# Kernel optimization log

Measured on AMD Instinct MI355X. Metric: run time of the kernel, lower is better.

## Reference

```python
import math
import jax, jax.numpy as jnp
import numpy as np

N_TOKENS = 131072
D_MODEL = 1024
NUM_EXPERT = 64
SWITCH_EPS = 0.1
CAP_RATE = 1.2  # training capacity factor


def setup_inputs() -> dict:
    key = jax.random.key(0)
    k1, k2, k3, k4 = jax.random.split(key, 4)
    inp = jax.random.normal(k1, (N_TOKENS, D_MODEL), dtype=jnp.float32)
    W = jax.random.normal(k2, (D_MODEL, NUM_EXPERT), dtype=jnp.float32) * (1.0 / math.sqrt(D_MODEL))
    b = jax.random.normal(k3, (NUM_EXPERT,), dtype=jnp.float32) * 0.01
    noise = jax.random.uniform(k4, (N_TOKENS, NUM_EXPERT), dtype=jnp.float32)
    return {"inp": inp, "W": W, "b": b, "noise": noise}


def reference(inp, W, b, noise):
    n_tokens = inp.shape[0]
    # gate projection + training-time noise injection (noise in [1-eps, 1+eps])
    score = inp @ W + b
    score = score + (noise * (2.0 * SWITCH_EPS) + (1.0 - SWITCH_EPS))
    score = jax.nn.softmax(score.astype(jnp.float32), axis=-1)  # [N, E]

    # top-1 selection
    top1_idx = jnp.argmax(score, axis=-1)  # [N] int
    top1_score = jnp.take_along_axis(score, top1_idx[:, None], axis=-1)  # [N, 1]
    top1_score = top1_score.astype(inp.dtype)

    # capacity-limited pruning: keep first `capacity` tokens per expert (in order)
    capacity = math.ceil(CAP_RATE * n_tokens / NUM_EXPERT)  # static
    onehot = jax.nn.one_hot(top1_idx, NUM_EXPERT, dtype=jnp.int32)  # [N, E]
    # rank of each token within its expert (0-based, tokens in arrival order)
    rank = jnp.sum(jnp.cumsum(onehot, axis=0) * onehot, axis=-1) - 1  # [N]
    pruned_idx = jnp.where(rank < capacity, top1_idx, -1)  # [N]

    # load-balancing loss over valid (non-pruned) assignments
    valid = pruned_idx > -1
    n_valid = jnp.sum(valid).astype(jnp.float32)
    safe_idx = jnp.where(valid, pruned_idx, 0)
    counts = jnp.zeros((NUM_EXPERT,), dtype=jnp.float32).at[safe_idx].add(valid.astype(jnp.float32))
    fraction_expert = counts / n_valid
    prob_expert = jnp.sum(score, axis=0) / n_valid
    loss = jnp.sum(fraction_expert * prob_expert) * NUM_EXPERT

    return pruned_idx[:, None], top1_score, loss
```

## Files before the change

kernel.cpp:

```cpp
#include <hip/hip_runtime.h>
#include <stdint.h>

#define NTOK   131072
#define DM     1024
#define NE     64
#define TB     64
#define NBLK   2048
#define BK     32
#define NCHUNK 32
#define CAP    2458
#define EPG    16

__device__ __forceinline__ void gload_lds16(const float* g, float* l) {
    __builtin_amdgcn_global_load_lds(
        (const __attribute__((address_space(1))) void*)g,
        (__attribute__((address_space(3))) void*)l, 16, 0, 0);
}

__global__ __launch_bounds__(256, 8)
void gate_kernel(const float* __restrict__ A, const float* __restrict__ W,
                 const float* __restrict__ bias, const float* __restrict__ noise,
                 float* __restrict__ out, int* __restrict__ pk,
                 int* __restrict__ histg, float* __restrict__ colpart)
{
    __shared__ float asA[2][TB][BK];
    __shared__ float smax[TB][5];
    __shared__ float ssum[TB][5];
    __shared__ int   sidx[TB][5];

    const int tid  = threadIdx.x;
    const int lane = tid & 63;
    const int wv   = __builtin_amdgcn_readfirstlane(tid >> 6);
    const int g16  = wv << 4;
    const int blk  = blockIdx.x;
    const int tokBase = blk * TB;
    const int token   = tokBase + lane;

    float acc[EPG];
#pragma unroll
    for (int e = 0; e < EPG; ++e) acc[e] = 0.f;

    const int sl = (lane & 7) ^ ((lane >> 3) & 7);
    const float* gsrc = A + (size_t)(tokBase + wv * 16 + (lane >> 3)) * DM + sl * 4;
    float* lb[2] = { &asA[0][wv * 16][0], &asA[1][wv * 16][0] };

    gload_lds16(gsrc,          lb[0]);
    gload_lds16(gsrc + 8 * DM, lb[0] + 8 * BK);
    __syncthreads();

#pragma unroll 1
    for (int c = 0; c < NCHUNK; ++c) {
        const int cur = c & 1;
        if (c + 1 < NCHUNK) {
            const float* gn = gsrc + (size_t)(c + 1) * BK;
            float* ln = lb[cur ^ 1];
            gload_lds16(gn,          ln);
            gload_lds16(gn + 8 * DM, ln + 8 * BK);
        }
        const float* arow = &asA[cur][lane][0];
        const int k0 = c * BK;
#pragma unroll
        for (int q = 0; q < 8; ++q) {
            const float4 xq = *(const float4*)(arow + ((q ^ (lane & 7)) << 2));
            const float xs[4] = {xq.x, xq.y, xq.z, xq.w};
#pragma unroll
            for (int kk = 0; kk < 4; ++kk) {
                const float x = xs[kk];
                const float* wrow = W + (size_t)(k0 + q * 4 + kk) * NE + g16;
#pragma unroll
                for (int e = 0; e < EPG; ++e)
                    acc[e] = fmaf(x, wrow[e], acc[e]);
            }
        }
        __syncthreads();
    }

    const float* nrow = noise + (size_t)token * NE + g16;
    const float* brow = bias + g16;
#pragma unroll
    for (int q = 0; q < 4; ++q) {
        const float4 nv = ((const float4*)nrow)[q];
        acc[q * 4 + 0] += brow[q * 4 + 0] + nv.x * 0.2f + 0.9f;
        acc[q * 4 + 1] += brow[q * 4 + 1] + nv.y * 0.2f + 0.9f;
        acc[q * 4 + 2] += brow[q * 4 + 2] + nv.z * 0.2f + 0.9f;
        acc[q * 4 + 3] += brow[q * 4 + 3] + nv.w * 0.2f + 0.9f;
    }

    float lm = acc[0]; int li = 0;
#pragma unroll
    for (int e = 1; e < EPG; ++e)
        if (acc[e] > lm) { lm = acc[e]; li = e; }
    smax[lane][wv] = lm;
    sidx[lane][wv] = g16 + li;
    __syncthreads();

    float M = smax[lane][0]; int bi = sidx[lane][0];
#pragma unroll
    for (int g2 = 1; g2 < 4; ++g2) {
        const float m2 = smax[lane][g2];
        if (m2 > M) { M = m2; bi = sidx[lane][g2]; }
    }

    float s = 0.f;
#pragma unroll
    for (int e = 0; e < EPG; ++e) { acc[e] = __expf(acc[e] - M); s += acc[e]; }
    ssum[lane][wv] = s;
    __syncthreads();
    const float denom = ssum[lane][0] + ssum[lane][1] + ssum[lane][2] + ssum[lane][3];
    const float inv = 1.0f / denom;
#pragma unroll
    for (int e = 0; e < EPG; ++e) acc[e] *= inv;

    if (wv == 0) out[NTOK + token] = inv;

#define XSTAGE(M_)                                                       \
    {                                                                    \
        const bool up_ = (lane & (M_)) != 0;                             \
        _Pragma("unroll")                                                \
        for (int j = 0; j < (M_); ++j) {                                 \
            const float a_ = acc[j], b_ = acc[j + (M_)];                 \
            const float r_ = __shfl_xor(up_ ? a_ : b_, (M_), 64);        \
            acc[j] = (up_ ? b_ : a_) + r_;                               \
        }                                                                \
    }
    XSTAGE(8) XSTAGE(4) XSTAGE(2) XSTAGE(1)
#undef XSTAGE
    float cs = acc[0];
    cs += __shfl_xor(cs, 16, 64);
    cs += __shfl_xor(cs, 32, 64);
    if (lane < EPG) colpart[blk * NE + g16 + lane] = cs;

    if (wv == 0) {
        const uint64_t below = (1ull << lane) - 1ull;
        int lrank = 0, h = 0;
#pragma unroll 1
        for (int e = 0; e < NE; ++e) {
            const uint64_t mb = __ballot(bi == e);
            if (bi == e)   lrank = (int)__popcll(mb & below);
            if (lane == e) h = (int)__popcll(mb);
        }
        pk[token] = bi | (lrank << 6);
        histg[blk * NE + lane] = h;
    }
}

__global__ void scan_kernel(int* __restrict__ hist, const float* __restrict__ colpart,
                            float* __restrict__ out)
{
    __shared__ int   segsum[4][NE];
    __shared__ float segcol[4][NE];
    const int tid = threadIdx.x;
    const int e   = tid & 63;
    const int seg = tid >> 6;
    const int b0  = seg * 512, b1 = b0 + 512;

    int s = 0; float cs = 0.f;
    for (int b = b0; b < b1; ++b) { s += hist[b * NE + e]; cs += colpart[b * NE + e]; }
    segsum[seg][e] = s;
    segcol[seg][e] = cs;
    __syncthreads();

    int run = 0;
    for (int w = 0; w < seg; ++w) run += segsum[w][e];
    for (int b = b0; b < b1; ++b) {
        const int h = hist[b * NE + e];
        hist[b * NE + e] = run;
        run += h;
    }

    if (tid < 64) {
        const int   total = segsum[0][e] + segsum[1][e] + segsum[2][e] + segsum[3][e];
        const float csum  = segcol[0][e] + segcol[1][e] + segcol[2][e] + segcol[3][e];
        const float cnt   = (float)((total < CAP) ? total : CAP);
        float nv = cnt;
        float contrib = cnt * csum;
#pragma unroll
        for (int m = 32; m; m >>= 1) {
            nv      += __shfl_xor(nv, m, 64);
            contrib += __shfl_xor(contrib, m, 64);
        }
        if (tid == 0) out[2 * NTOK] = 64.0f * contrib / (nv * nv);
    }
}

__global__ void finalize_kernel(const int* __restrict__ pk, const int* __restrict__ offs,
                                float* __restrict__ out)
{
    const int i = blockIdx.x * 256 + threadIdx.x;
    const int v = pk[i];
    const int e = v & 63;
    const int r = (v >> 6) + offs[(i >> 6) * NE + e];
    out[i] = (r < CAP) ? (float)e : -1.0f;
}

extern "C" void kernel_launch(void* const* d_in, const int* in_sizes, int n_in,
                              void* d_out, int out_size, void* d_ws, size_t ws_size,
                              hipStream_t stream)
{
    (void)in_sizes; (void)n_in; (void)out_size; (void)ws_size;
    const float* A     = (const float*)d_in[0];
    const float* W     = (const float*)d_in[1];
    const float* bias  = (const float*)d_in[2];
    const float* noise = (const float*)d_in[3];
    float* out = (float*)d_out;

    char* ws = (char*)d_ws;
    int*   pkbuf   = (int*)ws;
    int*   histg   = (int*)(ws + 524288);
    float* colpart = (float*)(ws + 2 * 524288);

    gate_kernel<<<NBLK, 256, 0, stream>>>(A, W, bias, noise, out, pkbuf, histg, colpart);
    scan_kernel<<<1, 256, 0, stream>>>(histg, colpart, out);
    finalize_kernel<<<NTOK / 256, 256, 0, stream>>>(pkbuf, histg, out);
}
```

Measured before the change: 265.8 us.

## Parallelize histogram scan across experts and refine gate pipeline barriers

The single-block serial scan over 2048 block histograms becomes a 64-block kernel, one block per expert, using wave shuffle prefix sums. The loss reduction moves into a separate tiny kernel. In the gate kernel, the double-buffered LDS loop now uses explicit s_barrier plus vmcnt waits, so the next chunk's global-to-LDS load stays in flight during compute. The cost is one extra kernel launch, and the barrier ordering adds correctness risk.

Result: faster. 252.7 us (-4.9%).

```diff
diff --git a/kernel.cpp b/kernel.cpp
--- a/kernel.cpp
+++ b/kernel.cpp
@@ -46,17 +46,25 @@
 
     gload_lds16(gsrc,          lb[0]);
     gload_lds16(gsrc + 8 * DM, lb[0] + 8 * BK);
-    __syncthreads();
 
 #pragma unroll 1
     for (int c = 0; c < NCHUNK; ++c) {
         const int cur = c & 1;
+        __builtin_amdgcn_s_barrier();
+        asm volatile("" ::: "memory");
         if (c + 1 < NCHUNK) {
             const float* gn = gsrc + (size_t)(c + 1) * BK;
             float* ln = lb[cur ^ 1];
             gload_lds16(gn,          ln);
             gload_lds16(gn + 8 * DM, ln + 8 * BK);
+            asm volatile("s_waitcnt vmcnt(2)" ::: "memory");
+        } else {
+            asm volatile("s_waitcnt vmcnt(0)" ::: "memory");
         }
+        __builtin_amdgcn_sched_barrier(0);
+        __builtin_amdgcn_s_barrier();
+        asm volatile("" ::: "memory");
+
         const float* arow = &asA[cur][lane][0];
         const int k0 = c * BK;
 #pragma unroll
@@ -72,8 +80,8 @@
                     acc[e] = fmaf(x, wrow[e], acc[e]);
             }
         }
-        __syncthreads();
-    }
+    }
+    __syncthreads();
 
     const float* nrow = noise + (size_t)token * NE + g16;
     const float* brow = bias + g16;
@@ -144,43 +152,65 @@
     }
 }
 
-__global__ void scan_kernel(int* __restrict__ hist, const float* __restrict__ colpart,
+__global__ __launch_bounds__(256)
+void scan_kernel(int* __restrict__ hist, const float* __restrict__ colpart,
+                 int* __restrict__ totals, float* __restrict__ colsums)
+{
+    __shared__ int   wtot[4];
+    __shared__ float wcs[4];
+    const int e    = blockIdx.x;
+    const int t    = threadIdx.x;
+    const int lane = t & 63;
+    const int w    = t >> 6;
+    const int b0   = t * 8;
+
+    int h[8]; int s = 0; float csl = 0.f;
+#pragma unroll
+    for (int i = 0; i < 8; ++i) {
+        h[i]  = hist[(b0 + i) * NE + e];
+        csl  += colpart[(b0 + i) * NE + e];
+        s    += h[i];
+    }
+    int inc = s;
+#pragma unroll
+    for (int d = 1; d < 64; d <<= 1) {
+        const int v = __shfl_up(inc, d, 64);
+        if (lane >= d) inc += v;
+    }
+    float wsum = csl;
+#pragma unroll
+    for (int m = 32; m; m >>= 1) wsum += __shfl_xor(wsum, m, 64);
+    if (lane == 63) wtot[w] = inc;
+    if (lane == 0)  wcs[w]  = wsum;
+    __syncthreads();
+
+    int base = 0;
+#pragma unroll
+    for (int ww = 0; ww < 4; ++ww) base += (ww < w) ? wtot[ww] : 0;
+    int run = base + inc - s;
+#pragma unroll
+    for (int i = 0; i < 8; ++i) { hist[(b0 + i) * NE + e] = run; run += h[i]; }
+
+    if (t == 0) {
+        totals[e]  = wtot[0] + wtot[1] + wtot[2] + wtot[3];
+        colsums[e] = wcs[0] + wcs[1] + wcs[2] + wcs[3];
+    }
+}
+
+__global__ void loss_kernel(const int* __restrict__ totals,
+                            const float* __restrict__ colsums,
                             float* __restrict__ out)
 {
-    __shared__ int   segsum[4][NE];
-    __shared__ float segcol[4][NE];
-    const int tid = threadIdx.x;
-    const int e   = tid & 63;
-    const int seg = tid >> 6;
-    const int b0  = seg * 512, b1 = b0 + 512;
-
-    int s = 0; float cs = 0.f;
-    for (int b = b0; b < b1; ++b) { s += hist[b * NE + e]; cs += colpart[b * NE + e]; }
-    segsum[seg][e] = s;
-    segcol[seg][e] = cs;
-    __syncthreads();
-
-    int run = 0;
-    for (int w = 0; w < seg; ++w) run += segsum[w][e];
-    for (int b = b0; b < b1; ++b) {
-        const int h = hist[b * NE + e];
-        hist[b * NE + e] = run;
-        run += h;
-    }
-
-    if (tid < 64) {
-        const int   total = segsum[0][e] + segsum[1][e] + segsum[2][e] + segsum[3][e];
-        const float csum  = segcol[0][e] + segcol[1][e] + segcol[2][e] + segcol[3][e];
-        const float cnt   = (float)((total < CAP) ? total : CAP);
-        float nv = cnt;
-        float contrib = cnt * csum;
-#pragma unroll
-        for (int m = 32; m; m >>= 1) {
-            nv      += __shfl_xor(nv, m, 64);
-            contrib += __shfl_xor(contrib, m, 64);
-        }
-        if (tid == 0) out[2 * NTOK] = 64.0f * contrib / (nv * nv);
-    }
+    const int e   = threadIdx.x;
+    const int tot = totals[e];
+    const float cnt = (float)((tot < CAP) ? tot : CAP);
+    float nv = cnt, contrib = cnt * colsums[e];
+#pragma unroll
+    for (int m = 32; m; m >>= 1) {
+        nv      += __shfl_xor(nv, m, 64);
+        contrib += __shfl_xor(contrib, m, 64);
+    }
+    if (e == 0) out[2 * NTOK] = 64.0f * contrib / (nv * nv);
 }
 
 __global__ void finalize_kernel(const int* __restrict__ pk, const int* __restrict__ offs,
@@ -208,8 +238,11 @@
     int*   pkbuf   = (int*)ws;
     int*   histg   = (int*)(ws + 524288);
     float* colpart = (float*)(ws + 2 * 524288);
+    int*   totals  = (int*)(ws + 3 * 524288);
+    float* colsums = (float*)(ws + 3 * 524288 + 256);
 
     gate_kernel<<<NBLK, 256, 0, stream>>>(A, W, bias, noise, out, pkbuf, histg, colpart);
-    scan_kernel<<<1, 256, 0, stream>>>(histg, colpart, out);
+    scan_kernel<<<NE, 256, 0, stream>>>(histg, colpart, totals, colsums);
+    loss_kernel<<<1, 64, 0, stream>>>(totals, colsums, out);
     finalize_kernel<<<NTOK / 256, 256, 0, stream>>>(pkbuf, histg, out);
 }
```
